# Kernel optimization log

Measured on AMD Instinct MI355X. Metric: run time of the kernel, lower is better.

The kernel has to match this reference:

```python
import jax, jax.numpy as jnp
import numpy as np

N_NODES = 50000
N_EDGES = 600000
D_FEAT = 128
NHID = 128
N_CLASSES = 40


def gcn_conv(x, W, b, src, dst, n_nodes):
    """PyG-style GCNConv: out = D^{-1/2} (A + I) D^{-1/2} (x W) + b.

    src/dst: [E'] edge endpoints including self-loops; messages are gathered
    from src and scatter-added at dst with symmetric normalization.
    """
    h = x @ W  # [N, out] -- transform before propagate (linearity => same math)
    deg = jax.ops.segment_sum(jnp.ones_like(dst, dtype=h.dtype), dst,
                              num_segments=n_nodes)  # in-degree incl. self-loop
    dinv = jnp.where(deg > 0, jax.lax.rsqrt(deg), 0.0)
    norm = dinv[src] * dinv[dst]  # [E']
    msg = h[src] * norm[:, None]  # [E', out] gather + scale
    out = jax.ops.segment_sum(msg, dst, num_segments=n_nodes)  # scatter-add
    return out + b


def setup_inputs() -> dict:
    key = jax.random.key(0)
    ks = jax.random.split(key, 8)
    x = jax.random.normal(ks[0], (N_NODES, D_FEAT), dtype=jnp.float32)
    edge_index = jax.random.randint(ks[1], (2, N_EDGES), 0, N_NODES, dtype=jnp.int64)
    # Glorot-ish scaled params
    W1 = jax.random.normal(ks[2], (D_FEAT, NHID), dtype=jnp.float32) / np.sqrt(D_FEAT)
    b1 = jnp.zeros((NHID,), dtype=jnp.float32)
    W2 = jax.random.normal(ks[3], (NHID, NHID), dtype=jnp.float32) / np.sqrt(NHID)
    b2 = jnp.zeros((NHID,), dtype=jnp.float32)
    Wlin = jax.random.normal(ks[4], (NHID, N_CLASSES), dtype=jnp.float32) / np.sqrt(NHID)
    blin = jnp.zeros((N_CLASSES,), dtype=jnp.float32)
    return {"x": x, "edge_index": edge_index, "W1": W1, "b1": b1,
            "W2": W2, "b2": b2, "Wlin": Wlin, "blin": blin}


def reference(x, edge_index, W1, b1, W2, b2, Wlin, blin):
    n = x.shape[0]
    loop = jnp.arange(n, dtype=edge_index.dtype)
    src = jnp.concatenate([edge_index[0], loop])  # add self-loops
    dst = jnp.concatenate([edge_index[1], loop])
    h = gcn_conv(x, W1, b1, src, dst, n)
    h = jnp.tanh(h)  # dropout is identity in eval mode
    h = gcn_conv(h, W2, b2, src, dst, n)
    h = jnp.tanh(h)
    return h @ Wlin + blin  # [N, num_classes]
```

## Files before the change

### kernel.cpp

```cpp
#include <hip/hip_runtime.h>
#include <cmath>

#define D 128
#define NCLS 40
#define GG 391
#define CAP 64

typedef __bf16 bfrag __attribute__((ext_vector_type(8)));
typedef float ffrag __attribute__((ext_vector_type(4)));
typedef unsigned int u32;
typedef unsigned int u32x4 __attribute__((ext_vector_type(4)));

__device__ inline float fast_tanh(float x) {
  float ax = __builtin_fabsf(x);
  float z = __expf(-2.0f * ax);
  float r = (1.0f - z) * __builtin_amdgcn_rcpf(1.0f + z);
  return copysignf(r, x);
}

__global__ __launch_bounds__(256) void zero_deg(int* __restrict__ deg, int N) {
  int i = blockIdx.x * 256 + threadIdx.x;
  if (i < N) deg[i] = 0;
}

__global__ __launch_bounds__(256) void mega1(const float* __restrict__ A, const float* __restrict__ W1,
                                             const float* __restrict__ W2, const float* __restrict__ Wl,
                                             __bf16* __restrict__ C, int N,
                                             const int* __restrict__ src, const int* __restrict__ dst, int E,
                                             int* __restrict__ deg, int* __restrict__ csr,
                                             __bf16* __restrict__ Wt2, __bf16* __restrict__ Wlt, int EB) {
  const int b = blockIdx.x;
  const int tid = threadIdx.x;
  if (b >= GG) {
    if (b < GG + EB) {
      int e = (b - GG) * 256 + tid;
      if (e < E) {
        int s = src[e], d = dst[e];
        int pos = atomicAdd(&deg[d], 1);
        if (pos < CAP) csr[d * CAP + pos] = s;
      }
    } else {
      int j = (b - GG - EB) * 256 + tid;
      if (j < 16384) {
        Wt2[j] = (__bf16)W2[(j & 127) * D + (j >> 7)];
      } else if (j < 16384 + 48 * D) {
        int q = j - 16384;
        int n = q >> 7, k = q & 127;
        Wlt[q] = (n < NCLS) ? (__bf16)Wl[k * NCLS + n] : (__bf16)0.0f;
      }
    }
    return;
  }
  __shared__ __align__(16) __bf16 Bs[128][136];
  const int wave = tid >> 6, lane = tid & 63;
  const int row0 = b * 128 + wave * 32;
  const int koff = (lane >> 4) * 8;

  for (int i = tid; i < 128 * 128; i += 256) {
    int n = i & 127, k = i >> 7;
    Bs[n][k] = (__bf16)W1[k * D + n];
  }

  bfrag a[2][4];
#pragma unroll
  for (int mt = 0; mt < 2; ++mt) {
    int r = row0 + mt * 16 + (lane & 15);
    int rc = r < N ? r : N - 1;
    const float* p = A + (size_t)rc * D;
#pragma unroll
    for (int kk = 0; kk < 4; ++kk) {
      float4 u = *(const float4*)(p + kk * 32 + koff);
      float4 v = *(const float4*)(p + kk * 32 + koff + 4);
      bfrag f;
      f[0] = (__bf16)u.x; f[1] = (__bf16)u.y; f[2] = (__bf16)u.z; f[3] = (__bf16)u.w;
      f[4] = (__bf16)v.x; f[5] = (__bf16)v.y; f[6] = (__bf16)v.z; f[7] = (__bf16)v.w;
      a[mt][kk] = f;
    }
  }
  __syncthreads();

  ffrag acc[2][8];
#pragma unroll
  for (int mt = 0; mt < 2; ++mt)
#pragma unroll
    for (int n = 0; n < 8; ++n) acc[mt][n] = (ffrag){0.f, 0.f, 0.f, 0.f};

#pragma unroll
  for (int kk = 0; kk < 4; ++kk) {
#pragma unroll
    for (int n = 0; n < 8; ++n) {
      bfrag bb = *(const bfrag*)(&Bs[n * 16 + (lane & 15)][kk * 32 + koff]);
      acc[0][n] = __builtin_amdgcn_mfma_f32_16x16x32_bf16(a[0][kk], bb, acc[0][n], 0, 0, 0);
      acc[1][n] = __builtin_amdgcn_mfma_f32_16x16x32_bf16(a[1][kk], bb, acc[1][n], 0, 0, 0);
    }
  }

  int ocol = lane & 15;
#pragma unroll
  for (int mt = 0; mt < 2; ++mt) {
    int orow0 = row0 + mt * 16 + (lane >> 4) * 4;
#pragma unroll
    for (int n = 0; n < 8; ++n)
#pragma unroll
      for (int i = 0; i < 4; ++i) {
        int r = orow0 + i;
        if (r < N) C[(size_t)r * D + n * 16 + ocol] = (__bf16)acc[mt][n][i];
      }
  }
}

__global__ __launch_bounds__(256) void scale_rows(__bf16* __restrict__ t, const int* __restrict__ deg, int N) {
  int i = blockIdx.x * 256 + threadIdx.x;
  int row = i >> 4;
  if (row >= N) return;
  float dv = rsqrtf((float)deg[row] + 1.0f);
  __bf16* p = t + (size_t)row * D + (i & 15) * 8;
  bfrag v = *(const bfrag*)p;
  bfrag o;
#pragma unroll
  for (int k = 0; k < 8; ++k) o[k] = (__bf16)(dv * (float)v[k]);
  *(bfrag*)p = o;
}

__device__ inline void gather16s(const __bf16* __restrict__ t, const int* __restrict__ deg,
                                 const int* __restrict__ csr, const float* __restrict__ bias,
                                 __bf16 (*Hs)[136], float* dvs, int node0, int wave, int lane, int N) {
  const int g = lane >> 4, sl = lane & 15;
  const int node = node0 + wave * 4 + g;
  const int nd = node < N ? node : N - 1;
  const int cnt = deg[nd];
  const int jm = cnt < CAP ? cnt : CAP;
  const float dv = rsqrtf((float)cnt + 1.0f);
  if (sl == 0) dvs[wave * 4 + g] = dv;

  int mx = jm;
  int o1 = __shfl_xor(mx, 16, 64);
  mx = mx > o1 ? mx : o1;
  int o2 = __shfl_xor(mx, 32, 64);
  mx = mx > o2 ? mx : o2;
  const int jmw = __builtin_amdgcn_readfirstlane(mx);

  bfrag tv = *(const bfrag*)(t + (size_t)nd * D + sl * 8);
  float acc[8];
#pragma unroll
  for (int i = 0; i < 8; ++i) acc[i] = (float)tv[i];

  for (int base = 0; base < jmw; base += 16) {
    int rem = jm - base;
    int es = nd;
    if (sl < rem) es = csr[nd * CAP + base + sl];
    int nin = jmw - base; nin = nin < 16 ? nin : 16;
    for (int j = 0; j < nin; ++j) {
      int s = __shfl(es, g * 16 + j, 64);
      bfrag r = *(const bfrag*)(t + (size_t)s * D + sl * 8);
      if (base + j < jm) {
#pragma unroll
        for (int i = 0; i < 8; ++i) acc[i] += (float)r[i];
      }
    }
  }

  float4 b0 = *(const float4*)(bias + sl * 8);
  float4 b1 = *(const float4*)(bias + sl * 8 + 4);
  bfrag o;
  o[0] = (__bf16)fast_tanh(dv * acc[0] + b0.x);
  o[1] = (__bf16)fast_tanh(dv * acc[1] + b0.y);
  o[2] = (__bf16)fast_tanh(dv * acc[2] + b0.z);
  o[3] = (__bf16)fast_tanh(dv * acc[3] + b0.w);
  o[4] = (__bf16)fast_tanh(dv * acc[4] + b1.x);
  o[5] = (__bf16)fast_tanh(dv * acc[5] + b1.y);
  o[6] = (__bf16)fast_tanh(dv * acc[6] + b1.z);
  o[7] = (__bf16)fast_tanh(dv * acc[7] + b1.w);
  *(u32x4*)&Hs[wave * 4 + g][sl * 8] = *(u32x4*)&o;
}

__global__ __launch_bounds__(256) void gather_gemm(const __bf16* __restrict__ t, const int* __restrict__ deg,
                                                   const int* __restrict__ csr, const float* __restrict__ bias,
                                                   const __bf16* __restrict__ Wt, __bf16* __restrict__ C, int N) {
  __shared__ __align__(16) __bf16 Hs[16][136];
  __shared__ float dvs[16];
  const int tid = threadIdx.x;
  const int wave = tid >> 6, lane = tid & 63;
  const int g = lane >> 4, sl = lane & 15;
  const int node0 = blockIdx.x * 16;

  gather16s(t, deg, csr, bias, Hs, dvs, node0, wave, lane, N);
  __syncthreads();

  const int koff = g * 8;
  bfrag a[4];
#pragma unroll
  for (int kk = 0; kk < 4; ++kk) a[kk] = *(const bfrag*)(&Hs[sl][kk * 32 + koff]);
  ffrag acc2[2];
  acc2[0] = (ffrag){0.f, 0.f, 0.f, 0.f};
  acc2[1] = (ffrag){0.f, 0.f, 0.f, 0.f};
#pragma unroll
  for (int nt = 0; nt < 2; ++nt) {
    const __bf16* wp = Wt + (size_t)(wave * 32 + nt * 16 + sl) * D;
    bfrag bfr[4];
#pragma unroll
    for (int kk = 0; kk < 4; ++kk) bfr[kk] = *(const bfrag*)(wp + kk * 32 + koff);
#pragma unroll
    for (int kk = 0; kk < 4; ++kk)
      acc2[nt] = __builtin_amdgcn_mfma_f32_16x16x32_bf16(a[kk], bfr[kk], acc2[nt], 0, 0, 0);
  }
#pragma unroll
  for (int nt = 0; nt < 2; ++nt) {
    int ccol = wave * 32 + nt * 16 + sl;
#pragma unroll
    for (int i = 0; i < 4; ++i) {
      int r = node0 + g * 4 + i;
      if (r < N) C[(size_t)r * D + ccol] = (__bf16)(dvs[g * 4 + i] * acc2[nt][i]);
    }
  }
}

__global__ __launch_bounds__(256) void gather_head(const __bf16* __restrict__ t, const int* __restrict__ deg,
                                                   const int* __restrict__ csr, const float* __restrict__ bias,
                                                   const __bf16* __restrict__ Wlt, const float* __restrict__ blin,
                                                   float* __restrict__ out, int N) {
  __shared__ __align__(16) __bf16 Hs[16][136];
  __shared__ float dvs[16];
  const int tid = threadIdx.x;
  const int wave = tid >> 6, lane = tid & 63;
  const int g = lane >> 4, sl = lane & 15;
  const int node0 = blockIdx.x * 16;

  gather16s(t, deg, csr, bias, Hs, dvs, node0, wave, lane, N);
  __syncthreads();

  if (wave < 3) {
    const int koff = g * 8;
    bfrag a[4];
#pragma unroll
    for (int kk = 0; kk < 4; ++kk) a[kk] = *(const bfrag*)(&Hs[sl][kk * 32 + koff]);
    ffrag acc2 = (ffrag){0.f, 0.f, 0.f, 0.f};
    const __bf16* wp = Wlt + (size_t)(wave * 16 + sl) * D;
    bfrag bfr[4];
#pragma unroll
    for (int kk = 0; kk < 4; ++kk) bfr[kk] = *(const bfrag*)(wp + kk * 32 + koff);
#pragma unroll
    for (int kk = 0; kk < 4; ++kk)
      acc2 = __builtin_amdgcn_mfma_f32_16x16x32_bf16(a[kk], bfr[kk], acc2, 0, 0, 0);

    int ccol = wave * 16 + sl;
    if (ccol < NCLS) {
      float bl = blin[ccol];
#pragma unroll
      for (int i = 0; i < 4; ++i) {
        int r = node0 + g * 4 + i;
        if (r < N) out[(size_t)r * NCLS + ccol] = acc2[i] + bl;
      }
    }
  }
}

extern "C" void kernel_launch(void* const* d_in, const int* in_sizes, int n_in,
                              void* d_out, int out_size, void* d_ws, size_t ws_size,
                              hipStream_t stream) {
  const float* x    = (const float*)d_in[0];
  const int*   ei   = (const int*)d_in[1];
  const float* W1   = (const float*)d_in[2];
  const float* b1   = (const float*)d_in[3];
  const float* W2   = (const float*)d_in[4];
  const float* b2   = (const float*)d_in[5];
  const float* Wlin = (const float*)d_in[6];
  const float* blin = (const float*)d_in[7];
  float* out = (float*)d_out;

  const int N = in_sizes[0] / D;
  const int E = in_sizes[1] / 2;
  const int* srcp = ei;
  const int* dstp = ei + E;

  char* ws = (char*)d_ws;
  int*    deg = (int*)ws;
  __bf16* Wt2 = (__bf16*)(ws + ((size_t)256 << 10));
  __bf16* Wlt = (__bf16*)(ws + ((size_t)320 << 10));
  int*    csr = (int*)(ws + ((size_t)1 << 20));
  __bf16* tb  = (__bf16*)(ws + ((size_t)16 << 20));
  __bf16* hb  = (__bf16*)(ws + ((size_t)32 << 20));

  const int nb = (N + 255) / 256;
  const int eb = (E + 255) / 256;
  const int cvb = (16384 + 48 * D + 255) / 256;
  const int gb = (N + 15) / 16;
  dim3 b256(256);

  zero_deg<<<nb, b256, 0, stream>>>(deg, N);
  mega1<<<GG + eb + cvb, b256, 0, stream>>>(x, W1, W2, Wlin, tb, N, srcp, dstp, E, deg, csr, Wt2, Wlt, eb);
  scale_rows<<<(N * 16 + 255) / 256, b256, 0, stream>>>(tb, deg, N);
  gather_gemm<<<gb, b256, 0, stream>>>(tb, deg, csr, b1, Wt2, hb, N);
  gather_head<<<gb, b256, 0, stream>>>(hb, deg, csr, b2, Wlt, blin, out, N);
}
```

Before: 185.3 us.

## Sort nodes by degree bucket so gather waves process similar-degree nodes

Builds a degree-bucketed permutation of the nodes with a counting sort: atomic slot assignment in scale_rows, then a prefix scan and scatter in a new perm_build kernel. The gather kernels then process nodes in permuted order and write results back to the original rows. The aim is to cut wave divergence, since each wave loops to the maximum in-degree among its four nodes. In exchange it adds a kernel launch and atomic contention on 64 bins, and loses contiguous row locality for node reads and output writes.

```diff
diff --git a/kernel.cpp b/kernel.cpp
--- a/kernel.cpp
+++ b/kernel.cpp
@@ -18,9 +18,19 @@
   return copysignf(r, x);
 }
 
-__global__ __launch_bounds__(256) void zero_deg(int* __restrict__ deg, int N) {
+__device__ inline int wave_incl_scan(int x, int lane) {
+#pragma unroll
+  for (int off = 1; off < 64; off <<= 1) {
+    int y = __shfl_up(x, off, 64);
+    if (lane >= off) x += y;
+  }
+  return x;
+}
+
+__global__ __launch_bounds__(256) void zero_deg(int* __restrict__ deg, int* __restrict__ bins, int N) {
   int i = blockIdx.x * 256 + threadIdx.x;
   if (i < N) deg[i] = 0;
+  if (blockIdx.x == 0 && threadIdx.x < 64) bins[threadIdx.x] = 0;
 }
 
 __global__ __launch_bounds__(256) void mega1(const float* __restrict__ A, const float* __restrict__ W1,
@@ -109,11 +119,17 @@
   }
 }
 
-__global__ __launch_bounds__(256) void scale_rows(__bf16* __restrict__ t, const int* __restrict__ deg, int N) {
+__global__ __launch_bounds__(256) void scale_rows(__bf16* __restrict__ t, const int* __restrict__ deg,
+                                                  int* __restrict__ bins, int* __restrict__ myslot, int N) {
   int i = blockIdx.x * 256 + threadIdx.x;
   int row = i >> 4;
   if (row >= N) return;
-  float dv = rsqrtf((float)deg[row] + 1.0f);
+  int dgv = deg[row];
+  if ((i & 15) == 0) {
+    int bkt = dgv < 63 ? dgv : 63;
+    myslot[row] = atomicAdd(&bins[bkt], 1);
+  }
+  float dv = rsqrtf((float)dgv + 1.0f);
   __bf16* p = t + (size_t)row * D + (i & 15) * 8;
   bfrag v = *(const bfrag*)p;
   bfrag o;
@@ -122,16 +138,36 @@
   *(bfrag*)p = o;
 }
 
+__global__ __launch_bounds__(256) void perm_build(const int* __restrict__ deg, const int* __restrict__ myslot,
+                                                  const int* __restrict__ bins, int* __restrict__ perm, int N) {
+  __shared__ int off[64];
+  const int tid = threadIdx.x;
+  if (tid < 64) {
+    int v = bins[tid];
+    int x = wave_incl_scan(v, tid);
+    off[tid] = x - v;
+  }
+  __syncthreads();
+  int i = blockIdx.x * 256 + tid;
+  if (i < N) {
+    int bkt = deg[i]; bkt = bkt < 63 ? bkt : 63;
+    perm[off[bkt] + myslot[i]] = i;
+  }
+}
+
 __device__ inline void gather16s(const __bf16* __restrict__ t, const int* __restrict__ deg,
                                  const int* __restrict__ csr, const float* __restrict__ bias,
-                                 __bf16 (*Hs)[136], float* dvs, int node0, int wave, int lane, int N) {
+                                 const int* __restrict__ perm,
+                                 __bf16 (*Hs)[136], float* dvs, int* pnds,
+                                 int node0, int wave, int lane, int N) {
   const int g = lane >> 4, sl = lane & 15;
-  const int node = node0 + wave * 4 + g;
-  const int nd = node < N ? node : N - 1;
+  int p = node0 + wave * 4 + g;
+  p = p < N ? p : N - 1;
+  const int nd = perm[p];
   const int cnt = deg[nd];
   const int jm = cnt < CAP ? cnt : CAP;
   const float dv = rsqrtf((float)cnt + 1.0f);
-  if (sl == 0) dvs[wave * 4 + g] = dv;
+  if (sl == 0) { dvs[wave * 4 + g] = dv; pnds[wave * 4 + g] = nd; }
 
   int mx = jm;
   int o1 = __shfl_xor(mx, 16, 64);
@@ -176,15 +212,17 @@
 
 __global__ __launch_bounds__(256) void gather_gemm(const __bf16* __restrict__ t, const int* __restrict__ deg,
                                                    const int* __restrict__ csr, const float* __restrict__ bias,
+                                                   const int* __restrict__ perm,
                                                    const __bf16* __restrict__ Wt, __bf16* __restrict__ C, int N) {
   __shared__ __align__(16) __bf16 Hs[16][136];
   __shared__ float dvs[16];
+  __shared__ int pnds[16];
   const int tid = threadIdx.x;
   const int wave = tid >> 6, lane = tid & 63;
   const int g = lane >> 4, sl = lane & 15;
   const int node0 = blockIdx.x * 16;
 
-  gather16s(t, deg, csr, bias, Hs, dvs, node0, wave, lane, N);
+  gather16s(t, deg, csr, bias, perm, Hs, dvs, pnds, node0, wave, lane, N);
   __syncthreads();
 
   const int koff = g * 8;
@@ -209,24 +247,26 @@
     int ccol = wave * 32 + nt * 16 + sl;
 #pragma unroll
     for (int i = 0; i < 4; ++i) {
-      int r = node0 + g * 4 + i;
-      if (r < N) C[(size_t)r * D + ccol] = (__bf16)(dvs[g * 4 + i] * acc2[nt][i]);
+      int r = pnds[g * 4 + i];
+      C[(size_t)r * D + ccol] = (__bf16)(dvs[g * 4 + i] * acc2[nt][i]);
     }
   }
 }
 
 __global__ __launch_bounds__(256) void gather_head(const __bf16* __restrict__ t, const int* __restrict__ deg,
                                                    const int* __restrict__ csr, const float* __restrict__ bias,
+                                                   const int* __restrict__ perm,
                                                    const __bf16* __restrict__ Wlt, const float* __restrict__ blin,
                                                    float* __restrict__ out, int N) {
   __shared__ __align__(16) __bf16 Hs[16][136];
   __shared__ float dvs[16];
+  __shared__ int pnds[16];
   const int tid = threadIdx.x;
   const int wave = tid >> 6, lane = tid & 63;
   const int g = lane >> 4, sl = lane & 15;
   const int node0 = blockIdx.x * 16;
 
-  gather16s(t, deg, csr, bias, Hs, dvs, node0, wave, lane, N);
+  gather16s(t, deg, csr, bias, perm, Hs, dvs, pnds, node0, wave, lane, N);
   __syncthreads();
 
   if (wave < 3) {
@@ -248,8 +288,8 @@
       float bl = blin[ccol];
 #pragma unroll
       for (int i = 0; i < 4; ++i) {
-        int r = node0 + g * 4 + i;
-        if (r < N) out[(size_t)r * NCLS + ccol] = acc2[i] + bl;
+        int r = pnds[g * 4 + i];
+        out[(size_t)r * NCLS + ccol] = acc2[i] + bl;
       }
     }
   }
@@ -274,12 +314,15 @@
   const int* dstp = ei + E;
 
   char* ws = (char*)d_ws;
-  int*    deg = (int*)ws;
-  __bf16* Wt2 = (__bf16*)(ws + ((size_t)256 << 10));
-  __bf16* Wlt = (__bf16*)(ws + ((size_t)320 << 10));
-  int*    csr = (int*)(ws + ((size_t)1 << 20));
-  __bf16* tb  = (__bf16*)(ws + ((size_t)16 << 20));
-  __bf16* hb  = (__bf16*)(ws + ((size_t)32 << 20));
+  int*    deg    = (int*)ws;
+  int*    myslot = (int*)(ws + ((size_t)256 << 10));
+  int*    bins   = (int*)(ws + ((size_t)472 << 10));
+  __bf16* Wt2    = (__bf16*)(ws + ((size_t)512 << 10));
+  __bf16* Wlt    = (__bf16*)(ws + ((size_t)560 << 10));
+  int*    perm   = (int*)(ws + ((size_t)640 << 10));
+  int*    csr    = (int*)(ws + ((size_t)1 << 20));
+  __bf16* tb     = (__bf16*)(ws + ((size_t)16 << 20));
+  __bf16* hb     = (__bf16*)(ws + ((size_t)32 << 20));
 
   const int nb = (N + 255) / 256;
   const int eb = (E + 255) / 256;
@@ -287,9 +330,10 @@
   const int gb = (N + 15) / 16;
   dim3 b256(256);
 
-  zero_deg<<<nb, b256, 0, stream>>>(deg, N);
+  zero_deg<<<nb, b256, 0, stream>>>(deg, bins, N);
   mega1<<<GG + eb + cvb, b256, 0, stream>>>(x, W1, W2, Wlin, tb, N, srcp, dstp, E, deg, csr, Wt2, Wlt, eb);
-  scale_rows<<<(N * 16 + 255) / 256, b256, 0, stream>>>(tb, deg, N);
-  gather_gemm<<<gb, b256, 0, stream>>>(tb, deg, csr, b1, Wt2, hb, N);
-  gather_head<<<gb, b256, 0, stream>>>(hb, deg, csr, b2, Wlt, blin, out, N);
-}
+  scale_rows<<<(N * 16 + 255) / 256, b256, 0, stream>>>(tb, deg, bins, myslot, N);
+  perm_build<<<nb, b256, 0, stream>>>(deg, myslot, bins, perm, N);
+  gather_gemm<<<gb, b256, 0, stream>>>(tb, deg, csr, b1, perm, Wt2, hb, N);
+  gather_head<<<gb, b256, 0, stream>>>(hb, deg, csr, b2, perm, Wlt, blin, out, N);
+}
```

After: 392.5 us. 2.12x slower.
